# Kernel optimization log

Measured on AMD Instinct MI355X. Metric: run time of the kernel, lower is better.

## Reference

```python
import jax, jax.numpy as jnp
import numpy as np

N_O = 50000
N_Q = 50000
E = 1_600_000
POS_DIM = 3
LATENT = 128
HEADS = 4
HEAD_DIM = 32
EDGE_IN = 3 * POS_DIM  # ['rel','q_pos','o_pos']


def setup_inputs() -> dict:
    key = jax.random.key(0)
    ks = jax.random.split(key, 12)
    h_obs = jax.random.normal(ks[0], (N_O, LATENT), dtype=jnp.float32)
    pos_obs = jax.random.uniform(ks[1], (N_O, POS_DIM), dtype=jnp.float32)
    pos_query = jax.random.uniform(ks[2], (N_Q, POS_DIM), dtype=jnp.float32)
    src = jax.random.randint(ks[3], (E,), 0, N_O, dtype=jnp.int32)
    dst = jnp.sort(jax.random.randint(ks[4], (E,), 0, N_Q, dtype=jnp.int32))
    s = 0.05
    W1 = jax.random.normal(ks[5], (EDGE_IN, LATENT), dtype=jnp.float32) * s
    b1 = jnp.zeros((LATENT,), dtype=jnp.float32)
    W2 = jax.random.normal(ks[6], (LATENT, HEADS), dtype=jnp.float32) * s
    b2 = jnp.zeros((HEADS,), dtype=jnp.float32)
    Wv = jax.random.normal(ks[7], (LATENT, HEADS * HEAD_DIM), dtype=jnp.float32) * s
    bv = jnp.zeros((HEADS * HEAD_DIM,), dtype=jnp.float32)
    log_sigma = jnp.float32(-2.0)
    return {"h_obs": h_obs, "pos_obs": pos_obs, "pos_query": pos_query,
            "src": src, "dst": dst,
            "W1": W1, "b1": b1, "W2": W2, "b2": b2,
            "Wv": Wv, "bv": bv, "log_sigma": log_sigma}


def _forward(h_obs, pos_obs, pos_query, src, dst, W1, b1, W2, b2, Wv, bv, log_sigma):
    pos_o = pos_obs[src]                      # [E, P]
    pos_q = pos_query[dst]                    # [E, P]
    rel = pos_q - pos_o
    edge_attr = jnp.concatenate([rel, pos_q, pos_o], axis=-1)   # [E, 3P]
    hid = jax.nn.relu(edge_attr @ W1 + b1)                      # [E, LATENT]
    logits = hid @ W2 + b2                                      # [E, H]
    dist2 = jnp.sum(rel * rel, axis=-1, keepdims=True)          # [E, 1]
    sigma = jnp.exp(log_sigma) + 1e-6
    logits = logits - dist2 / (2.0 * sigma * sigma)             # kernel log-weight
    # segment softmax over edges grouped by dst
    n_q = pos_query.shape[0]
    m = jax.ops.segment_max(logits, dst, num_segments=n_q)      # [N_q, H]
    ex = jnp.exp(logits - m[dst])
    denom = jax.ops.segment_sum(ex, dst, num_segments=n_q)      # [N_q, H]
    attn = ex / (denom[dst] + 1e-16)                            # [E, H]
    v = (h_obs @ Wv + bv).reshape(-1, HEADS, HEAD_DIM)          # [N_o, H, D]
    msg = attn[:, :, None] * v[src]                             # [E, H, D]
    out = jax.ops.segment_sum(msg, dst, num_segments=n_q)       # [N_q, H, D]
    return out.reshape(n_q, HEADS * HEAD_DIM)


def reference(h_obs, pos_obs, pos_query, src, dst, W1, b1, W2, b2, Wv, bv, log_sigma):
    return _forward(h_obs, pos_obs, pos_query, src, dst, W1, b1, W2, b2, Wv, bv, log_sigma)
```

## Files before the change

kernel.cpp:

```cpp
#include <hip/hip_runtime.h>
#include <hip/hip_bf16.h>
#include <cstdint>
#include <cstddef>

#define N_O 50000
#define N_Q 50000
#define NE  1600000

#define EDGE_BLOCKS  (NE / 128)
#define VP_BLOCKS    ((N_O + 63) / 64)
#define RP_BLOCKS    ((N_Q + 256) / 256)
#define WCAP 264

typedef __attribute__((ext_vector_type(8)))  short short8;
typedef __attribute__((ext_vector_type(16))) float f32x16;

__device__ inline unsigned short f2bf(float x) {
    __hip_bfloat16 hb = __float2bfloat16(x);
    return *reinterpret_cast<unsigned short*>(&hb);
}

__global__ void pack_kernel(const float* __restrict__ W1, const float* __restrict__ b1,
                            const float* __restrict__ W2, const float* __restrict__ b2,
                            const float* __restrict__ log_sigma,
                            unsigned short* __restrict__ W1cT,
                            unsigned short* __restrict__ W2tb,
                            float* __restrict__ scal) {
    int j = threadIdx.x;
    if (j < 128) {
        #pragma unroll
        for (int a = 0; a < 3; ++a) {
            W1cT[j * 8 + a]     = f2bf(W1[(3 + a) * 128 + j] + W1[a * 128 + j]);
            W1cT[j * 8 + 3 + a] = f2bf(W1[(6 + a) * 128 + j] - W1[a * 128 + j]);
        }
        W1cT[j * 8 + 6] = f2bf(b1[j]);
        W1cT[j * 8 + 7] = 0;
        #pragma unroll
        for (int hd = 0; hd < 4; ++hd)
            W2tb[hd * 128 + j] = f2bf(W2[j * 4 + hd]);
    } else if (j == 128) {
        float sigma = expf(log_sigma[0]) + 1e-6f;
        scal[0] = 1.0f / (2.0f * sigma * sigma);
        scal[1] = b2[0]; scal[2] = b2[1]; scal[3] = b2[2]; scal[4] = b2[3];
    }
}

__device__ void rowptr_body(int bid, const int* __restrict__ dst, int* __restrict__ rp) {
    int q = bid * 256 + threadIdx.x;
    if (q > N_Q) return;
    int lo = 0, hi = NE;
    while (lo < hi) {
        int mid = (lo + hi) >> 1;
        if (dst[mid] < q) lo = mid + 1; else hi = mid;
    }
    rp[q] = lo;
}

__device__ void vproj_body(int bid, const float* __restrict__ h,
                           const float* __restrict__ Wv,
                           const float* __restrict__ bv,
                           unsigned short* __restrict__ v,
                           float* Ash ) {
    int t = threadIdx.x;
    int n0 = bid * 64;
    #pragma unroll
    for (int rep = 0; rep < 8; ++rep) {
        int idx = rep * 256 + t;
        int row = idx >> 5, c4 = (idx & 31) * 4;
        float4 val = make_float4(0.f, 0.f, 0.f, 0.f);
        if (n0 + row < N_O) val = *(const float4*)(h + (size_t)(n0 + row) * 128 + c4);
        float* d = &Ash[row * 132 + c4];
        d[0] = val.x; d[1] = val.y; d[2] = val.z; d[3] = val.w;
    }
    __syncthreads();

    int cg = t & 15, rg = t >> 4;
    int c0 = cg * 8, r0 = rg * 4;
    float acc[4][8];
    #pragma unroll
    for (int i = 0; i < 4; ++i)
        #pragma unroll
        for (int j = 0; j < 8; ++j) acc[i][j] = 0.f;

    const float4* Wv4 = (const float4*)Wv;
    for (int k = 0; k < 128; ++k) {
        float4 b0 = Wv4[k * 32 + cg * 2];
        float4 b1v = Wv4[k * 32 + cg * 2 + 1];
        float bb[8] = {b0.x, b0.y, b0.z, b0.w, b1v.x, b1v.y, b1v.z, b1v.w};
        #pragma unroll
        for (int i = 0; i < 4; ++i) {
            float a = Ash[(r0 + i) * 132 + k];
            #pragma unroll
            for (int j = 0; j < 8; ++j) acc[i][j] += a * bb[j];
        }
    }

    float bvv[8];
    #pragma unroll
    for (int j = 0; j < 8; ++j) bvv[j] = bv[c0 + j];
    #pragma unroll
    for (int i = 0; i < 4; ++i) {
        int n = n0 + r0 + i;
        if (n < N_O) {
            uint4 o;
            __hip_bfloat162 t0 = __float22bfloat162_rn(
                make_float2(acc[i][0] + bvv[0], acc[i][1] + bvv[1]));
            __hip_bfloat162 t1 = __float22bfloat162_rn(
                make_float2(acc[i][2] + bvv[2], acc[i][3] + bvv[3]));
            __hip_bfloat162 t2 = __float22bfloat162_rn(
                make_float2(acc[i][4] + bvv[4], acc[i][5] + bvv[5]));
            __hip_bfloat162 t3 = __float22bfloat162_rn(
                make_float2(acc[i][6] + bvv[6], acc[i][7] + bvv[7]));
            o.x = *reinterpret_cast<unsigned int*>(&t0);
            o.y = *reinterpret_cast<unsigned int*>(&t1);
            o.z = *reinterpret_cast<unsigned int*>(&t2);
            o.w = *reinterpret_cast<unsigned int*>(&t3);
            *(uint4*)(v + (size_t)n * 128 + c0) = o;
        }
    }
}

__device__ void edge_body(int bid, const float* __restrict__ pos_obs,
                          const float* __restrict__ pos_query,
                          const int* __restrict__ src,
                          const int* __restrict__ dst,
                          const unsigned short* __restrict__ W1cT,
                          const unsigned short* __restrict__ W2tb,
                          const float* __restrict__ scal,
                          float* __restrict__ logitsT,
                          unsigned char* smem ) {
    int t = threadIdx.x;
    int wave = t >> 6, lane = t & 63;
    int i = lane & 31, h = lane >> 5;
    unsigned char* myrow = smem + wave * 8448 + i * 264;

    short8 zero8;
    #pragma unroll
    for (int k = 0; k < 8; ++k) zero8[k] = 0;

    short8 a1[4];
    #pragma unroll
    for (int b = 0; b < 4; ++b)
        a1[b] = (h == 0) ? *(const short8*)(W1cT + (32 * b + i) * 8) : zero8;

    short8 a2[8];
    #pragma unroll
    for (int m = 0; m < 8; ++m)
        a2[m] = (i < 4) ? *(const short8*)(W2tb + i * 128 + m * 16 + h * 8) : zero8;

    int e = bid * 128 + wave * 32 + i;
    int s = src[e], d = dst[e];
    float pox = pos_obs[s * 3 + 0], poy = pos_obs[s * 3 + 1], poz = pos_obs[s * 3 + 2];
    float pqx = pos_query[d * 3 + 0], pqy = pos_query[d * 3 + 1], pqz = pos_query[d * 3 + 2];
    float rx = pqx - pox, ry = pqy - poy, rz = pqz - poz;
    float dist2 = rx * rx + ry * ry + rz * rz;

    short8 bea = zero8;
    if (h == 0) {
        bea[0] = (short)f2bf(pqx); bea[1] = (short)f2bf(pqy); bea[2] = (short)f2bf(pqz);
        bea[3] = (short)f2bf(pox); bea[4] = (short)f2bf(poy); bea[5] = (short)f2bf(poz);
        bea[6] = (short)0x3F80;
        bea[7] = 0;
    }

    f32x16 c1[4];
    #pragma unroll
    for (int b = 0; b < 4; ++b) {
        #pragma unroll
        for (int k = 0; k < 16; ++k) c1[b][k] = 0.0f;
        c1[b] = __builtin_amdgcn_mfma_f32_32x32x16_bf16(a1[b], bea, c1[b], 0, 0, 0);
    }

    #pragma unroll
    for (int b = 0; b < 4; ++b) {
        #pragma unroll
        for (int s_ = 0; s_ < 4; ++s_) {
            float x0 = fmaxf(c1[b][4 * s_ + 0], 0.f);
            float x1 = fmaxf(c1[b][4 * s_ + 1], 0.f);
            float x2 = fmaxf(c1[b][4 * s_ + 2], 0.f);
            float x3 = fmaxf(c1[b][4 * s_ + 3], 0.f);
            __hip_bfloat162 p0 = __float22bfloat162_rn(make_float2(x0, x1));
            __hip_bfloat162 p1 = __float22bfloat162_rn(make_float2(x2, x3));
            uint2 w;
            w.x = *reinterpret_cast<unsigned int*>(&p0);
            w.y = *reinterpret_cast<unsigned int*>(&p1);
            *(uint2*)(myrow + 64 * b + 16 * s_ + 8 * h) = w;
        }
    }

    f32x16 c2;
    #pragma unroll
    for (int k = 0; k < 16; ++k) c2[k] = 0.0f;
    #pragma unroll
    for (int m = 0; m < 8; ++m) {
        uint2 lo = *(const uint2*)(myrow + 32 * m + 16 * h);
        uint2 hi = *(const uint2*)(myrow + 32 * m + 16 * h + 8);
        union { unsigned int u[4]; short8 s; } bf;
        bf.u[0] = lo.x; bf.u[1] = lo.y; bf.u[2] = hi.x; bf.u[3] = hi.y;
        c2 = __builtin_amdgcn_mfma_f32_32x32x16_bf16(a2[m], bf.s, c2, 0, 0, 0);
    }

    if (h == 0) {
        float pen = dist2 * scal[0];
        logitsT[0 * NE + e] = c2[0] + scal[1] - pen;
        logitsT[1 * NE + e] = c2[1] + scal[2] - pen;
        logitsT[2 * NE + e] = c2[2] + scal[3] - pen;
        logitsT[3 * NE + e] = c2[3] + scal[4] - pen;
    }
}

__global__ __launch_bounds__(256) void fused_kernel(const float* __restrict__ pos_obs,
                                                    const float* __restrict__ pos_query,
                                                    const int* __restrict__ src,
                                                    const int* __restrict__ dst,
                                                    const unsigned short* __restrict__ W1cT,
                                                    const unsigned short* __restrict__ W2tb,
                                                    const float* __restrict__ scal,
                                                    float* __restrict__ logitsT,
                                                    const float* __restrict__ h_obs,
                                                    const float* __restrict__ Wv,
                                                    const float* __restrict__ bv,
                                                    unsigned short* __restrict__ vbuf,
                                                    int* __restrict__ rp) {
    __shared__ __align__(16) unsigned char smem[33792];
    int b = blockIdx.x;
    if (b < EDGE_BLOCKS) {
        edge_body(b, pos_obs, pos_query, src, dst, W1cT, W2tb, scal, logitsT, smem);
    } else if (b < EDGE_BLOCKS + VP_BLOCKS) {
        vproj_body(b - EDGE_BLOCKS, h_obs, Wv, bv, vbuf, (float*)smem);
    } else {
        rowptr_body(b - EDGE_BLOCKS - VP_BLOCKS, dst, rp);
    }
}

__global__ __launch_bounds__(256) void attn_kernel(const __hip_bfloat162* __restrict__ vb,
                                                   const float* __restrict__ logitsT,
                                                   const int* __restrict__ src,
                                                   const int* __restrict__ rp,
                                                   float* __restrict__ out) {
    __shared__ __align__(16) float wsh[4 * 4 * WCAP];
    int t = threadIdx.x;
    int lane = t & 63, wave = t >> 6;
    int q = blockIdx.x * 4 + wave;
    int s0 = rp[q], s1 = rp[q + 1];
    int cnt = s1 - s0;
    int h = lane >> 4, i = lane & 15;
    const float* lp = logitsT + (size_t)h * NE;

    float m = -INFINITY;
    for (int e = s0 + i; e < s1; e += 16) m = fmaxf(m, lp[e]);
    #pragma unroll
    for (int off = 8; off; off >>= 1) m = fmaxf(m, __shfl_xor(m, off));

    float acc0 = 0.f, acc1 = 0.f, r;

    if (cnt <= 256) {
        int s0a = s0 & ~3;
        float* wpb = wsh + wave * (4 * WCAP) + h * WCAP;
        float sum = 0.f;
        for (int e = s0 + i; e < s1; e += 16) {
            float w = __expf(lp[e] - m);
            wpb[e - s0a] = w;
            sum += w;
        }
        #pragma unroll
        for (int off = 8; off; off >>= 1) sum += __shfl_xor(sum, off);
        r = 1.0f / (sum + 1e-16f);

        int e = s0;
        int e1 = (s0 + 3) & ~3; if (e1 > s1) e1 = s1;
        for (; e < e1; ++e) {
            float w = wpb[e - s0a];
            float2 f = __bfloat1622float2(vb[(size_t)src[e] * 64 + lane]);
            acc0 += w * f.x; acc1 += w * f.y;
        }
        for (; e + 4 <= s1; e += 4) {
            float4 w4 = *(const float4*)(wpb + (e - s0a));
            int4 s4 = *(const int4*)(src + e);
            float2 f0 = __bfloat1622float2(vb[(size_t)s4.x * 64 + lane]);
            float2 f1 = __bfloat1622float2(vb[(size_t)s4.y * 64 + lane]);
            float2 f2 = __bfloat1622float2(vb[(size_t)s4.z * 64 + lane]);
            float2 f3 = __bfloat1622float2(vb[(size_t)s4.w * 64 + lane]);
            acc0 += w4.x * f0.x + w4.y * f1.x + w4.z * f2.x + w4.w * f3.x;
            acc1 += w4.x * f0.y + w4.y * f1.y + w4.z * f2.y + w4.w * f3.y;
        }
        for (; e < s1; ++e) {
            float w = wpb[e - s0a];
            float2 f = __bfloat1622float2(vb[(size_t)src[e] * 64 + lane]);
            acc0 += w * f.x; acc1 += w * f.y;
        }
    } else {
        float sum = 0.f;
        for (int e = s0 + i; e < s1; e += 16) sum += __expf(lp[e] - m);
        #pragma unroll
        for (int off = 8; off; off >>= 1) sum += __shfl_xor(sum, off);
        r = 1.0f / (sum + 1e-16f);

        int e = s0;
        for (; e < s1 && (e & 3); ++e) {
            float w = __expf(lp[e] - m);
            float2 f = __bfloat1622float2(vb[(size_t)src[e] * 64 + lane]);
            acc0 += w * f.x; acc1 += w * f.y;
        }
        for (; e + 4 <= s1; e += 4) {
            float4 l4 = *(const float4*)(lp + e);
            int4 s4 = *(const int4*)(src + e);
            float w0 = __expf(l4.x - m);
            float w1 = __expf(l4.y - m);
            float w2 = __expf(l4.z - m);
            float w3 = __expf(l4.w - m);
            float2 f0 = __bfloat1622float2(vb[(size_t)s4.x * 64 + lane]);
            float2 f1 = __bfloat1622float2(vb[(size_t)s4.y * 64 + lane]);
            float2 f2 = __bfloat1622float2(vb[(size_t)s4.z * 64 + lane]);
            float2 f3 = __bfloat1622float2(vb[(size_t)s4.w * 64 + lane]);
            acc0 += w0 * f0.x + w1 * f1.x + w2 * f2.x + w3 * f3.x;
            acc1 += w0 * f0.y + w1 * f1.y + w2 * f2.y + w3 * f3.y;
        }
        for (; e < s1; ++e) {
            float w = __expf(lp[e] - m);
            float2 f = __bfloat1622float2(vb[(size_t)src[e] * 64 + lane]);
            acc0 += w * f.x; acc1 += w * f.y;
        }
    }
    *(float2*)(out + (size_t)q * 128 + lane * 2) = make_float2(acc0 * r, acc1 * r);
}

extern "C" void kernel_launch(void* const* d_in, const int* in_sizes, int n_in,
                              void* d_out, int out_size, void* d_ws, size_t ws_size,
                              hipStream_t stream) {
    const float* h_obs     = (const float*)d_in[0];
    const float* pos_obs   = (const float*)d_in[1];
    const float* pos_query = (const float*)d_in[2];
    const int*   src       = (const int*)d_in[3];
    const int*   dst       = (const int*)d_in[4];
    const float* W1        = (const float*)d_in[5];
    const float* b1        = (const float*)d_in[6];
    const float* W2        = (const float*)d_in[7];
    const float* b2        = (const float*)d_in[8];
    const float* Wv        = (const float*)d_in[9];
    const float* bv        = (const float*)d_in[10];
    const float* log_sigma = (const float*)d_in[11];
    float* out = (float*)d_out;

    char* ws = (char*)d_ws;
    int*            rp      = (int*)(ws + 0);
    float*          scal    = (float*)(ws + 200192);
    unsigned short* W1cT    = (unsigned short*)(ws + 200256);
    unsigned short* W2tb    = (unsigned short*)(ws + 202304);
    unsigned short* vbuf    = (unsigned short*)(ws + 208640);
    float*          logitsT = (float*)(ws + 13008768);

    hipLaunchKernelGGL(pack_kernel, dim3(1), dim3(256), 0, stream,
                       W1, b1, W2, b2, log_sigma, W1cT, W2tb, scal);
    hipLaunchKernelGGL(fused_kernel, dim3(EDGE_BLOCKS + VP_BLOCKS + RP_BLOCKS),
                       dim3(256), 0, stream,
                       pos_obs, pos_query, src, dst, W1cT, W2tb, scal, logitsT,
                       h_obs, Wv, bv, vbuf, rp);
    hipLaunchKernelGGL(attn_kernel, dim3(N_Q / 4), dim3(256), 0, stream,
                       (const __hip_bfloat162*)vbuf, logitsT, src, rp, out);
}
```

Before: 249.1 us.

## Split edge MLP into its own 128-thread kernel with smaller shared memory

Pulls the edge-MLP path out of the combined fused kernel into a dedicated edge_kernel that uses 128-thread blocks and 16.9 KB of shared memory. The value projection and row-pointer work go into a separate fusedVR_kernel. Previously every block reserved 33 KB of LDS, sized for the vproj branch, which capped how many edge blocks could be resident per CU. The split should raise edge-kernel occupancy, at the cost of one extra launch and losing the overlap of vproj work with edge work.

```diff
diff --git a/kernel.cpp b/kernel.cpp
--- a/kernel.cpp
+++ b/kernel.cpp
@@ -7,7 +7,7 @@
 #define N_Q 50000
 #define NE  1600000
 
-#define EDGE_BLOCKS  (NE / 128)
+#define EDGE_BLOCKS  (NE / 64)
 #define VP_BLOCKS    ((N_O + 63) / 64)
 #define RP_BLOCKS    ((N_Q + 256) / 256)
 #define WCAP 264
@@ -120,15 +120,27 @@
     }
 }
 
-__device__ void edge_body(int bid, const float* __restrict__ pos_obs,
-                          const float* __restrict__ pos_query,
-                          const int* __restrict__ src,
-                          const int* __restrict__ dst,
-                          const unsigned short* __restrict__ W1cT,
-                          const unsigned short* __restrict__ W2tb,
-                          const float* __restrict__ scal,
-                          float* __restrict__ logitsT,
-                          unsigned char* smem ) {
+__global__ __launch_bounds__(256) void fusedVR_kernel(
+        const int* __restrict__ dst,
+        const float* __restrict__ h_obs, const float* __restrict__ Wv,
+        const float* __restrict__ bv, unsigned short* __restrict__ vbuf,
+        int* __restrict__ rp) {
+    __shared__ __align__(16) float Ash[64 * 132];
+    int b = blockIdx.x;
+    if (b < VP_BLOCKS) {
+        vproj_body(b, h_obs, Wv, bv, vbuf, Ash);
+    } else {
+        rowptr_body(b - VP_BLOCKS, dst, rp);
+    }
+}
+
+__global__ __launch_bounds__(128) void edge_kernel(
+        const float* __restrict__ pos_obs, const float* __restrict__ pos_query,
+        const int* __restrict__ src, const int* __restrict__ dst,
+        const unsigned short* __restrict__ W1cT,
+        const unsigned short* __restrict__ W2tb,
+        const float* __restrict__ scal, float* __restrict__ logitsT) {
+    __shared__ __align__(16) unsigned char smem[2 * 8448];
     int t = threadIdx.x;
     int wave = t >> 6, lane = t & 63;
     int i = lane & 31, h = lane >> 5;
@@ -148,7 +160,7 @@
     for (int m = 0; m < 8; ++m)
         a2[m] = (i < 4) ? *(const short8*)(W2tb + i * 128 + m * 16 + h * 8) : zero8;
 
-    int e = bid * 128 + wave * 32 + i;
+    int e = blockIdx.x * 64 + wave * 32 + i;
     int s = src[e], d = dst[e];
     float pox = pos_obs[s * 3 + 0], poy = pos_obs[s * 3 + 1], poz = pos_obs[s * 3 + 2];
     float pqx = pos_query[d * 3 + 0], pqy = pos_query[d * 3 + 1], pqz = pos_query[d * 3 + 2];
@@ -206,30 +218,6 @@
         logitsT[1 * NE + e] = c2[1] + scal[2] - pen;
         logitsT[2 * NE + e] = c2[2] + scal[3] - pen;
         logitsT[3 * NE + e] = c2[3] + scal[4] - pen;
-    }
-}
-
-__global__ __launch_bounds__(256) void fused_kernel(const float* __restrict__ pos_obs,
-                                                    const float* __restrict__ pos_query,
-                                                    const int* __restrict__ src,
-                                                    const int* __restrict__ dst,
-                                                    const unsigned short* __restrict__ W1cT,
-                                                    const unsigned short* __restrict__ W2tb,
-                                                    const float* __restrict__ scal,
-                                                    float* __restrict__ logitsT,
-                                                    const float* __restrict__ h_obs,
-                                                    const float* __restrict__ Wv,
-                                                    const float* __restrict__ bv,
-                                                    unsigned short* __restrict__ vbuf,
-                                                    int* __restrict__ rp) {
-    __shared__ __align__(16) unsigned char smem[33792];
-    int b = blockIdx.x;
-    if (b < EDGE_BLOCKS) {
-        edge_body(b, pos_obs, pos_query, src, dst, W1cT, W2tb, scal, logitsT, smem);
-    } else if (b < EDGE_BLOCKS + VP_BLOCKS) {
-        vproj_body(b - EDGE_BLOCKS, h_obs, Wv, bv, vbuf, (float*)smem);
-    } else {
-        rowptr_body(b - EDGE_BLOCKS - VP_BLOCKS, dst, rp);
     }
 }
 
@@ -352,10 +340,10 @@
 
     hipLaunchKernelGGL(pack_kernel, dim3(1), dim3(256), 0, stream,
                        W1, b1, W2, b2, log_sigma, W1cT, W2tb, scal);
-    hipLaunchKernelGGL(fused_kernel, dim3(EDGE_BLOCKS + VP_BLOCKS + RP_BLOCKS),
-                       dim3(256), 0, stream,
-                       pos_obs, pos_query, src, dst, W1cT, W2tb, scal, logitsT,
-                       h_obs, Wv, bv, vbuf, rp);
+    hipLaunchKernelGGL(fusedVR_kernel, dim3(VP_BLOCKS + RP_BLOCKS), dim3(256), 0, stream,
+                       dst, h_obs, Wv, bv, vbuf, rp);
+    hipLaunchKernelGGL(edge_kernel, dim3(EDGE_BLOCKS), dim3(128), 0, stream,
+                       pos_obs, pos_query, src, dst, W1cT, W2tb, scal, logitsT);
     hipLaunchKernelGGL(attn_kernel, dim3(N_Q / 4), dim3(256), 0, stream,
                        (const __hip_bfloat162*)vbuf, logitsT, src, rp, out);
 }
```

Result: no change. 249.0 us (-0.1%).
